# Optimization experiments

Hardware: AMD Instinct MI355X
Metric: run time of the kernel (lower is better)

The kernel has to match this reference:

```python
import jax, jax.numpy as jnp
import numpy as np

ALPHA_LEAKY = 0.2
EPS = 1e-10


def setup_inputs() -> dict:
    key = jax.random.key(0)
    ks = jax.random.split(key, 7)
    Nq, Nk, E, D = 100000, 100000, 1600000, 64
    return {
        "query_nodes": jax.random.normal(ks[0], (Nq, D), dtype=jnp.float32),
        "key_value_nodes": jax.random.normal(ks[1], (Nk, D), dtype=jnp.float32),
        "edge_index": jax.random.randint(ks[2], (2, E), 0, Nq, dtype=jnp.int64),
        "proj_w": jax.random.normal(ks[3], (D, D), dtype=jnp.float32) * 0.1,
        "proj_b": jax.random.normal(ks[4], (D,), dtype=jnp.float32) * 0.1,
        "attend_w": jax.random.normal(ks[5], (1, 2 * D), dtype=jnp.float32) * 0.1,
        "attend_b": jax.random.normal(ks[6], (1,), dtype=jnp.float32) * 0.1,
    }


def reference(query_nodes, key_value_nodes, edge_index, proj_w, proj_b, attend_w, attend_b):
    Nq, D = query_nodes.shape
    qi, ki = edge_index[0], edge_index[1]  # [E], [E]
    # per-edge gathered + projected features (torch Linear: x @ W.T + b)
    query_proj = query_nodes[qi] @ proj_w.T + proj_b      # [E, D]
    kv_proj = key_value_nodes[ki] @ proj_w.T + proj_b     # [E, D]
    # attend(concat([qp, kp])) == qp @ Wq.T + kp @ Wk.T + b  (avoids [E,2D] concat)
    wq, wk = attend_w[:, :D], attend_w[:, D:]
    e = query_proj @ wq[0] + kv_proj @ wk[0] + attend_b[0]  # [E]
    e = jax.nn.leaky_relu(e, negative_slope=ALPHA_LEAKY)
    # segment-wise (per query node) numerically-stable softmax
    e_max = jax.ops.segment_max(e, qi, num_segments=Nq)    # [Nq] (-inf for empty)
    e_exp = jnp.exp(e - e_max[qi])                          # [E]
    e_sum = jax.ops.segment_sum(e_exp, qi, num_segments=Nq)  # [Nq]
    attention = e_exp / (e_sum[qi] + EPS)                   # [E]  (dropout = identity in eval)
    # weighted scatter-add aggregation back to query nodes
    weighted_values = kv_proj * attention[:, None]          # [E, D]
    aggregated_context = jax.ops.segment_sum(weighted_values, qi, num_segments=Nq)  # [Nq, D]
    return aggregated_context
```

## Files before the change

### kernel.cpp

```cpp
#include <hip/hip_runtime.h>

#define ALPHA_LEAKY 0.2f
#define EPS_F 1e-10f

#define BSHIFT 7
#define BRANGE 128
#define NBMAX 1024
#define CHUNK_F 4096
#define KBUF_CAP 3072

using half4_t = __attribute__((ext_vector_type(4))) _Float16;
using f32x4 = __attribute__((ext_vector_type(4))) float;

__device__ __forceinline__ unsigned short f2bf(float x) {
  unsigned int u = __float_as_uint(x);
  return (unsigned short)((u + 0x7fffu + ((u >> 16) & 1u)) >> 16);
}

__global__ __launch_bounds__(256) void bin_proj_kernel(
    const int* __restrict__ eq, const int* __restrict__ ek,
    int* __restrict__ gcursor, unsigned int* __restrict__ pairs, int E,
    int NB, int binBlocks,
    const float* __restrict__ qnodes, const float* __restrict__ kvnodes,
    const float* __restrict__ W, const float* __restrict__ pb,
    const float* __restrict__ aw, unsigned int* __restrict__ Kp16,
    float* __restrict__ sq, float* __restrict__ sk,
    int Nq, int Nk, int projBlocks) {
  const int t = threadIdx.x;
  const bool isBin = (blockIdx.x % 5) == 0;

  if (isBin) {
    const int bb = blockIdx.x / 5;
    __shared__ int lcnt[NBMAX];
    __shared__ int lbase[NBMAX];
    for (int i = t; i < NBMAX; i += 256) lcnt[i] = 0;
    __syncthreads();

    const int cbase = bb * CHUNK_F;
    int4 qv[4], kv[4];
#pragma unroll
    for (int j = 0; j < 4; ++j) {
      const int e0 = cbase + (((j << 8) + t) << 2);
      if (e0 + 3 < E) {
        qv[j] = *(const int4*)(eq + e0);
        kv[j] = *(const int4*)(ek + e0);
      } else {
        int tq[4] = {-1, -1, -1, -1}, tk[4] = {0, 0, 0, 0};
        for (int r = 0; r < 4; ++r)
          if (e0 + r < E) { tq[r] = eq[e0 + r]; tk[r] = ek[e0 + r]; }
        qv[j] = make_int4(tq[0], tq[1], tq[2], tq[3]);
        kv[j] = make_int4(tk[0], tk[1], tk[2], tk[3]);
      }
      if (qv[j].x >= 0) atomicAdd(&lcnt[qv[j].x >> BSHIFT], 1);
      if (qv[j].y >= 0) atomicAdd(&lcnt[qv[j].y >> BSHIFT], 1);
      if (qv[j].z >= 0) atomicAdd(&lcnt[qv[j].z >> BSHIFT], 1);
      if (qv[j].w >= 0) atomicAdd(&lcnt[qv[j].w >> BSHIFT], 1);
    }
    __syncthreads();
    for (int i = t; i < NB; i += 256) {
      lbase[i] = lcnt[i] ? atomicAdd(&gcursor[i], lcnt[i]) : 0;
      lcnt[i] = 0;
    }
    __syncthreads();
#pragma unroll
    for (int j = 0; j < 4; ++j) {
      const int qs[4] = {qv[j].x, qv[j].y, qv[j].z, qv[j].w};
      const int ks[4] = {kv[j].x, kv[j].y, kv[j].z, kv[j].w};
#pragma unroll
      for (int r = 0; r < 4; ++r) {
        if (qs[r] >= 0) {
          const int b = qs[r] >> BSHIFT;
          const int idx = lbase[b] + atomicAdd(&lcnt[b], 1);
          if (idx < KBUF_CAP)
            pairs[(size_t)b * KBUF_CAP + idx] =
                ((unsigned int)(qs[r] & (BRANGE - 1)) << 20) |
                (unsigned int)ks[r];
        }
      }
    }
    return;
  }

  __shared__ float pt0[256];
  __shared__ __align__(16) float us[64];
  __shared__ float cq_s;
  const int lane = t & 63;
  const int projId = blockIdx.x - blockIdx.x / 5 - 1;
  const int waveId = projId * 4 + (t >> 6);
  const int nWaves = projBlocks * 4;

  {
    const int pd = t & 63, og = t >> 6;
    float s0 = 0.f;
#pragma unroll
    for (int oo = 0; oo < 16; ++oo) {
      const int o = og * 16 + oo;
      s0 = fmaf(aw[o], W[o * 64 + pd], s0);
    }
    pt0[t] = s0;
  }
  __syncthreads();
  if (t < 64) {
    us[t] = (pt0[t] + pt0[t + 64]) + (pt0[t + 128] + pt0[t + 192]);
    if (t == 0) {
      float c0 = 0.f;
      for (int o = 0; o < 64; ++o) c0 = fmaf(aw[o], pb[o], c0);
      cq_s = c0;
    }
  }
  __syncthreads();

  {
    const int sub = lane & 15, ng = lane >> 4;
    const float4 uv = ((const float4*)us)[sub];
    const float c = cq_s;
    for (int base = waveId * 4; base < Nq; base += nWaves * 4) {
      const int n = base + ng;
      float s = 0.f;
      if (n < Nq) {
        const float4 x = *(const float4*)(qnodes + (size_t)n * 64 + sub * 4);
        s = x.x * uv.x + x.y * uv.y + x.z * uv.z + x.w * uv.w;
      }
#pragma unroll
      for (int off = 1; off <= 8; off <<= 1) s += __shfl_xor(s, off, 64);
      if (sub == 0 && n < Nq) sq[n] = s + c;
    }
  }

  const int c = lane & 15, g = lane >> 4;

  half4_t Bf[4][4];
  float pbv[4];
#pragma unroll
  for (int nt = 0; nt < 4; ++nt) {
    pbv[nt] = pb[nt * 16 + c];
#pragma unroll
    for (int ks = 0; ks < 4; ++ks) {
      const float4 wv =
          *(const float4*)(W + (size_t)(nt * 16 + c) * 64 + ks * 16 + g * 4);
      half4_t h;
      h[0] = (_Float16)wv.x;
      h[1] = (_Float16)wv.y;
      h[2] = (_Float16)wv.z;
      h[3] = (_Float16)wv.w;
      Bf[nt][ks] = h;
    }
  }
  const float a0 = aw[64 + c], a1 = aw[80 + c], a2 = aw[96 + c],
              a3 = aw[112 + c];

  const int ntiles = (Nk + 15) >> 4;
  for (int tile = waveId; tile < ntiles; tile += nWaves) {
    const int n0 = tile << 4;
    const int arow = n0 + c;
    const bool aok = arow < Nk;
    const float* xr = kvnodes + (size_t)arow * 64 + g * 4;

    half4_t Af[4];
#pragma unroll
    for (int ks = 0; ks < 4; ++ks) {
      const float4 xv =
          aok ? *(const float4*)(xr + ks * 16) : make_float4(0.f, 0.f, 0.f, 0.f);
      half4_t h;
      h[0] = (_Float16)xv.x;
      h[1] = (_Float16)xv.y;
      h[2] = (_Float16)xv.z;
      h[3] = (_Float16)xv.w;
      Af[ks] = h;
    }

    f32x4 acc0 = {pbv[0], pbv[0], pbv[0], pbv[0]};
    f32x4 acc1 = {pbv[1], pbv[1], pbv[1], pbv[1]};
    f32x4 acc2 = {pbv[2], pbv[2], pbv[2], pbv[2]};
    f32x4 acc3 = {pbv[3], pbv[3], pbv[3], pbv[3]};
#pragma unroll
    for (int ks = 0; ks < 4; ++ks) {
      acc0 = __builtin_amdgcn_mfma_f32_16x16x16f16(Af[ks], Bf[0][ks], acc0, 0, 0, 0);
      acc1 = __builtin_amdgcn_mfma_f32_16x16x16f16(Af[ks], Bf[1][ks], acc1, 0, 0, 0);
      acc2 = __builtin_amdgcn_mfma_f32_16x16x16f16(Af[ks], Bf[2][ks], acc2, 0, 0, 0);
      acc3 = __builtin_amdgcn_mfma_f32_16x16x16f16(Af[ks], Bf[3][ks], acc3, 0, 0, 0);
    }

#pragma unroll
    for (int r = 0; r < 4; ++r) {
      const int node = n0 + g * 4 + r;
      if (node < Nk) {
        const unsigned int u0 =
            ((unsigned int)f2bf(acc1[r]) << 16) | f2bf(acc0[r]);
        const unsigned int u1 =
            ((unsigned int)f2bf(acc3[r]) << 16) | f2bf(acc2[r]);
        unsigned int* kp = Kp16 + (size_t)node * 32;
        kp[c] = u0;
        kp[16 + c] = u1;
      }
    }

    float ws0 = acc0[0] * a0 + acc1[0] * a1 + acc2[0] * a2 + acc3[0] * a3;
    float ws1 = acc0[1] * a0 + acc1[1] * a1 + acc2[1] * a2 + acc3[1] * a3;
    float ws2 = acc0[2] * a0 + acc1[2] * a1 + acc2[2] * a2 + acc3[2] * a3;
    float ws3 = acc0[3] * a0 + acc1[3] * a1 + acc2[3] * a2 + acc3[3] * a3;
#pragma unroll
    for (int off = 1; off <= 8; off <<= 1) {
      ws0 += __shfl_xor(ws0, off, 64);
      ws1 += __shfl_xor(ws1, off, 64);
      ws2 += __shfl_xor(ws2, off, 64);
      ws3 += __shfl_xor(ws3, off, 64);
    }
    if (c == 0) {
      const int nb4 = n0 + g * 4;
      if (nb4 + 3 < Nk) {
        *(float4*)(sk + nb4) = make_float4(ws0, ws1, ws2, ws3);
      } else {
        if (nb4 + 0 < Nk) sk[nb4 + 0] = ws0;
        if (nb4 + 1 < Nk) sk[nb4 + 1] = ws1;
        if (nb4 + 2 < Nk) sk[nb4 + 2] = ws2;
        if (nb4 + 3 < Nk) sk[nb4 + 3] = ws3;
      }
    }
  }
}

__global__ __launch_bounds__(512, 6) void sort_agg_kernel(
    const unsigned int* __restrict__ pairs, const int* __restrict__ gcursor,
    const float* __restrict__ sq, const float* __restrict__ sk,
    const float* __restrict__ ab, const unsigned int* __restrict__ Kp16,
    float* __restrict__ out, int Nq) {
  __shared__ int lcnt[BRANGE];
  __shared__ int lcur[BRANGE];
  __shared__ int lstart[BRANGE + 1];
  __shared__ int kibuf[KBUF_CAP];
  __shared__ int wso2[2];

  const int t = threadIdx.x;
  const int b = blockIdx.x;
  const int qlo = b << BSHIFT;
  int n = gcursor[b];
  if (n > KBUF_CAP) n = KBUF_CAP;
  const size_t base = (size_t)b * KBUF_CAP;

  if (t < BRANGE) lcnt[t] = 0;
  __syncthreads();

  unsigned int pv[6];
  int np = 0;
#pragma unroll
  for (int r = 0; r < 6; ++r) {
    const int i = t + (r << 9);
    if (i < n) { pv[r] = pairs[base + i]; ++np; }
  }
#pragma unroll
  for (int r = 0; r < 6; ++r)
    if (r < np) atomicAdd(&lcnt[pv[r] >> 20], 1);
  __syncthreads();

  const int lane = t & 63, wv = t >> 6;
  int v = 0, x = 0;
  if (t < BRANGE) {
    v = lcnt[t];
    x = v;
#pragma unroll
    for (int off = 1; off < 64; off <<= 1) {
      const int y = __shfl_up(x, off, 64);
      if (lane >= off) x += y;
    }
    if (lane == 63) wso2[wv] = x;
  }
  __syncthreads();
  if (t < BRANGE) {
    const int excl = ((wv == 1) ? wso2[0] : 0) + x - v;
    lstart[t] = excl;
    lcur[t] = excl;
    if (t == BRANGE - 1) lstart[BRANGE] = excl + v;
  }
  __syncthreads();

#pragma unroll
  for (int r = 0; r < 6; ++r)
    if (r < np)
      kibuf[atomicAdd(&lcur[pv[r] >> 20], 1)] = (int)(pv[r] & 0xFFFFFu);
  __syncthreads();

  const int ng = lane >> 3, dg = lane & 7;
  const float abv = ab[0];
#pragma unroll
  for (int pass = 0; pass < 2; ++pass) {
    const int l = (pass << 6) + (wv << 3) + ng;
    const int node = qlo + l;
    const bool act = node < Nq;
    const int s = act ? lstart[l] : 0;
    const int e = act ? lstart[l + 1] : 0;
    const float sqn = act ? sq[node] + abv : 0.f;

    float acc[8] = {0.f, 0.f, 0.f, 0.f, 0.f, 0.f, 0.f, 0.f};
    float wsum = 0.f;
    const int jm = e - 1;
#pragma unroll 1
    for (int j = s; j < e; j += 4) {
      const int ka = kibuf[j];
      const int kb = kibuf[min(j + 1, jm)];
      const int kc = kibuf[min(j + 2, jm)];
      const int kd = kibuf[min(j + 3, jm)];
      const float ea = sk[ka];
      const float eb = sk[kb];
      const float ec = sk[kc];
      const float ed = sk[kd];
      const uint4 ua = *(const uint4*)(Kp16 + (size_t)ka * 32 + (dg << 2));
      const uint4 ub = *(const uint4*)(Kp16 + (size_t)kb * 32 + (dg << 2));
      const uint4 uc = *(const uint4*)(Kp16 + (size_t)kc * 32 + (dg << 2));
      const uint4 ud = *(const uint4*)(Kp16 + (size_t)kd * 32 + (dg << 2));

      float xa = sqn + ea; xa = xa > 0.f ? xa : ALPHA_LEAKY * xa;
      float xb = sqn + eb; xb = xb > 0.f ? xb : ALPHA_LEAKY * xb;
      float xc = sqn + ec; xc = xc > 0.f ? xc : ALPHA_LEAKY * xc;
      float xd = sqn + ed; xd = xd > 0.f ? xd : ALPHA_LEAKY * xd;
      const float wa = __expf(xa);
      const float wb = (j + 1 < e) ? __expf(xb) : 0.f;
      const float wc = (j + 2 < e) ? __expf(xc) : 0.f;
      const float wd = (j + 3 < e) ? __expf(xd) : 0.f;

#define ACC8(W, U)                                             \
  acc[0] = fmaf(W, __uint_as_float(U.x << 16), acc[0]);        \
  acc[1] = fmaf(W, __uint_as_float(U.x & 0xffff0000u), acc[1]);\
  acc[2] = fmaf(W, __uint_as_float(U.y << 16), acc[2]);        \
  acc[3] = fmaf(W, __uint_as_float(U.y & 0xffff0000u), acc[3]);\
  acc[4] = fmaf(W, __uint_as_float(U.z << 16), acc[4]);        \
  acc[5] = fmaf(W, __uint_as_float(U.z & 0xffff0000u), acc[5]);\
  acc[6] = fmaf(W, __uint_as_float(U.w << 16), acc[6]);        \
  acc[7] = fmaf(W, __uint_as_float(U.w & 0xffff0000u), acc[7]);
      ACC8(wa, ua)
      ACC8(wb, ub)
      ACC8(wc, uc)
      ACC8(wd, ud)
#undef ACC8
      wsum += (wa + wb) + (wc + wd);
    }

    if (act) {
      const float inv = 1.0f / (wsum + EPS_F);
      const int obase = ((dg & 3) << 2) + ((dg >> 2) << 5);
      float4 r0 = {acc[0] * inv, acc[2] * inv, acc[4] * inv, acc[6] * inv};
      float4 r1 = {acc[1] * inv, acc[3] * inv, acc[5] * inv, acc[7] * inv};
      float* o = out + (size_t)node * 64 + obase;
      *(float4*)o = r0;
      *(float4*)(o + 16) = r1;
    }
  }
}

extern "C" void kernel_launch(void* const* d_in, const int* in_sizes, int n_in,
                              void* d_out, int out_size, void* d_ws, size_t ws_size,
                              hipStream_t stream) {
  const float* qnodes = (const float*)d_in[0];
  const float* kvnodes = (const float*)d_in[1];
  const int* ei = (const int*)d_in[2];
  const float* W = (const float*)d_in[3];
  const float* pb = (const float*)d_in[4];
  const float* aw = (const float*)d_in[5];
  const float* ab = (const float*)d_in[6];

  const int Nq = in_sizes[0] / 64;
  const int Nk = in_sizes[1] / 64;
  const int E = in_sizes[2] / 2;
  const int NB = (Nq + BRANGE - 1) >> BSHIFT;

  const int* eq = ei;
  const int* ek = ei + E;

  char* ws = (char*)d_ws;
  unsigned int* pairs = (unsigned int*)ws;
  unsigned int* Kp16 = pairs + (size_t)NBMAX * KBUF_CAP;
  float* sq = (float*)(Kp16 + (size_t)Nk * 32);
  float* sk = sq + Nq;
  int* gcursor = (int*)(sk + Nk);

  hipMemsetAsync(gcursor, 0, NBMAX * sizeof(int), stream);

  const int binBlocks = (E + CHUNK_F - 1) / CHUNK_F;
  const int projBlocks = binBlocks * 4;
  bin_proj_kernel<<<binBlocks * 5, 256, 0, stream>>>(
      eq, ek, gcursor, pairs, E, NB, binBlocks, qnodes, kvnodes, W, pb, aw,
      Kp16, sq, sk, Nq, Nk, projBlocks);

  sort_agg_kernel<<<NB, 512, 0, stream>>>(pairs, gcursor, sq, sk, ab, Kp16,
                                          (float*)d_out, Nq);
}
```

Before: 178.2 us.

## Split fused bin/projection kernel into separate launches and pad global bin counters

The combined kernel that interleaved binning blocks with projection blocks is split into a dedicated bin kernel (1024 threads, 16K-edge chunks) and a separate projection kernel with a fixed grid of 1664 blocks. Larger bin chunks mean far fewer global atomicAdds on the per-bin cursors. The cursors are also strided by 16 ints so each sits on its own cache line, reducing contention. In exchange there is an extra kernel launch and the binning and projection work no longer overlap inside one grid.

```diff
diff --git a/kernel.cpp b/kernel.cpp
--- a/kernel.cpp
+++ b/kernel.cpp
@@ -6,8 +6,9 @@
 #define BSHIFT 7
 #define BRANGE 128
 #define NBMAX 1024
-#define CHUNK_F 4096
+#define CHUNK_B 16384
 #define KBUF_CAP 3072
+#define GC_STRIDE 16
 
 using half4_t = __attribute__((ext_vector_type(4))) _Float16;
 using f32x4 = __attribute__((ext_vector_type(4))) float;
@@ -17,76 +18,72 @@
   return (unsigned short)((u + 0x7fffu + ((u >> 16) & 1u)) >> 16);
 }
 
-__global__ __launch_bounds__(256) void bin_proj_kernel(
+__global__ __launch_bounds__(1024) void bin_kernel(
     const int* __restrict__ eq, const int* __restrict__ ek,
     int* __restrict__ gcursor, unsigned int* __restrict__ pairs, int E,
-    int NB, int binBlocks,
+    int NB) {
+  __shared__ int lcnt[NBMAX];
+  __shared__ int lbase[NBMAX];
+  const int t = threadIdx.x;
+  for (int i = t; i < NBMAX; i += 1024) lcnt[i] = 0;
+  __syncthreads();
+
+  const int cbase = blockIdx.x * CHUNK_B;
+  int4 qv[4], kv[4];
+#pragma unroll
+  for (int j = 0; j < 4; ++j) {
+    const int e0 = cbase + (((j << 10) + t) << 2);
+    if (e0 + 3 < E) {
+      qv[j] = *(const int4*)(eq + e0);
+      kv[j] = *(const int4*)(ek + e0);
+    } else {
+      int tq[4] = {-1, -1, -1, -1}, tk[4] = {0, 0, 0, 0};
+      for (int r = 0; r < 4; ++r)
+        if (e0 + r < E) { tq[r] = eq[e0 + r]; tk[r] = ek[e0 + r]; }
+      qv[j] = make_int4(tq[0], tq[1], tq[2], tq[3]);
+      kv[j] = make_int4(tk[0], tk[1], tk[2], tk[3]);
+    }
+    if (qv[j].x >= 0) atomicAdd(&lcnt[qv[j].x >> BSHIFT], 1);
+    if (qv[j].y >= 0) atomicAdd(&lcnt[qv[j].y >> BSHIFT], 1);
+    if (qv[j].z >= 0) atomicAdd(&lcnt[qv[j].z >> BSHIFT], 1);
+    if (qv[j].w >= 0) atomicAdd(&lcnt[qv[j].w >> BSHIFT], 1);
+  }
+  __syncthreads();
+  for (int i = t; i < NB; i += 1024) {
+    lbase[i] = lcnt[i] ? atomicAdd(&gcursor[i * GC_STRIDE], lcnt[i]) : 0;
+    lcnt[i] = 0;
+  }
+  __syncthreads();
+#pragma unroll
+  for (int j = 0; j < 4; ++j) {
+    const int qs[4] = {qv[j].x, qv[j].y, qv[j].z, qv[j].w};
+    const int ks[4] = {kv[j].x, kv[j].y, kv[j].z, kv[j].w};
+#pragma unroll
+    for (int r = 0; r < 4; ++r) {
+      if (qs[r] >= 0) {
+        const int b = qs[r] >> BSHIFT;
+        const int idx = lbase[b] + atomicAdd(&lcnt[b], 1);
+        if (idx < KBUF_CAP)
+          pairs[(size_t)b * KBUF_CAP + idx] =
+              ((unsigned int)(qs[r] & (BRANGE - 1)) << 20) |
+              (unsigned int)ks[r];
+      }
+    }
+  }
+}
+
+__global__ __launch_bounds__(256) void proj_kernel(
     const float* __restrict__ qnodes, const float* __restrict__ kvnodes,
     const float* __restrict__ W, const float* __restrict__ pb,
     const float* __restrict__ aw, unsigned int* __restrict__ Kp16,
     float* __restrict__ sq, float* __restrict__ sk,
     int Nq, int Nk, int projBlocks) {
   const int t = threadIdx.x;
-  const bool isBin = (blockIdx.x % 5) == 0;
-
-  if (isBin) {
-    const int bb = blockIdx.x / 5;
-    __shared__ int lcnt[NBMAX];
-    __shared__ int lbase[NBMAX];
-    for (int i = t; i < NBMAX; i += 256) lcnt[i] = 0;
-    __syncthreads();
-
-    const int cbase = bb * CHUNK_F;
-    int4 qv[4], kv[4];
-#pragma unroll
-    for (int j = 0; j < 4; ++j) {
-      const int e0 = cbase + (((j << 8) + t) << 2);
-      if (e0 + 3 < E) {
-        qv[j] = *(const int4*)(eq + e0);
-        kv[j] = *(const int4*)(ek + e0);
-      } else {
-        int tq[4] = {-1, -1, -1, -1}, tk[4] = {0, 0, 0, 0};
-        for (int r = 0; r < 4; ++r)
-          if (e0 + r < E) { tq[r] = eq[e0 + r]; tk[r] = ek[e0 + r]; }
-        qv[j] = make_int4(tq[0], tq[1], tq[2], tq[3]);
-        kv[j] = make_int4(tk[0], tk[1], tk[2], tk[3]);
-      }
-      if (qv[j].x >= 0) atomicAdd(&lcnt[qv[j].x >> BSHIFT], 1);
-      if (qv[j].y >= 0) atomicAdd(&lcnt[qv[j].y >> BSHIFT], 1);
-      if (qv[j].z >= 0) atomicAdd(&lcnt[qv[j].z >> BSHIFT], 1);
-      if (qv[j].w >= 0) atomicAdd(&lcnt[qv[j].w >> BSHIFT], 1);
-    }
-    __syncthreads();
-    for (int i = t; i < NB; i += 256) {
-      lbase[i] = lcnt[i] ? atomicAdd(&gcursor[i], lcnt[i]) : 0;
-      lcnt[i] = 0;
-    }
-    __syncthreads();
-#pragma unroll
-    for (int j = 0; j < 4; ++j) {
-      const int qs[4] = {qv[j].x, qv[j].y, qv[j].z, qv[j].w};
-      const int ks[4] = {kv[j].x, kv[j].y, kv[j].z, kv[j].w};
-#pragma unroll
-      for (int r = 0; r < 4; ++r) {
-        if (qs[r] >= 0) {
-          const int b = qs[r] >> BSHIFT;
-          const int idx = lbase[b] + atomicAdd(&lcnt[b], 1);
-          if (idx < KBUF_CAP)
-            pairs[(size_t)b * KBUF_CAP + idx] =
-                ((unsigned int)(qs[r] & (BRANGE - 1)) << 20) |
-                (unsigned int)ks[r];
-        }
-      }
-    }
-    return;
-  }
-
   __shared__ float pt0[256];
   __shared__ __align__(16) float us[64];
   __shared__ float cq_s;
   const int lane = t & 63;
-  const int projId = blockIdx.x - blockIdx.x / 5 - 1;
-  const int waveId = projId * 4 + (t >> 6);
+  const int waveId = blockIdx.x * 4 + (t >> 6);
   const int nWaves = projBlocks * 4;
 
   {
@@ -234,7 +231,7 @@
   const int t = threadIdx.x;
   const int b = blockIdx.x;
   const int qlo = b << BSHIFT;
-  int n = gcursor[b];
+  int n = gcursor[b * GC_STRIDE];
   if (n > KBUF_CAP) n = KBUF_CAP;
   const size_t base = (size_t)b * KBUF_CAP;
 
@@ -373,13 +370,15 @@
   float* sk = sq + Nq;
   int* gcursor = (int*)(sk + Nk);
 
-  hipMemsetAsync(gcursor, 0, NBMAX * sizeof(int), stream);
-
-  const int binBlocks = (E + CHUNK_F - 1) / CHUNK_F;
-  const int projBlocks = binBlocks * 4;
-  bin_proj_kernel<<<binBlocks * 5, 256, 0, stream>>>(
-      eq, ek, gcursor, pairs, E, NB, binBlocks, qnodes, kvnodes, W, pb, aw,
-      Kp16, sq, sk, Nq, Nk, projBlocks);
+  hipMemsetAsync(gcursor, 0, NBMAX * GC_STRIDE * sizeof(int), stream);
+
+  const int binBlocks = (E + CHUNK_B - 1) / CHUNK_B;
+  bin_kernel<<<binBlocks, 1024, 0, stream>>>(eq, ek, gcursor, pairs, E, NB);
+
+  const int projBlocks = 1664;
+  proj_kernel<<<projBlocks, 256, 0, stream>>>(qnodes, kvnodes, W, pb, aw,
+                                              Kp16, sq, sk, Nq, Nk,
+                                              projBlocks);
 
   sort_agg_kernel<<<NB, 512, 0, stream>>>(pairs, gcursor, sq, sk, ab, Kp16,
                                           (float*)d_out, Nq);
```

Measured after the change: 185.1 us. 1.04x slower.
